# Kernel tuning notes

Hardware: AMD Instinct MI355X
Metric: run time of the kernel (lower is better)

Reference implementation:

```python
import jax, jax.numpy as jnp
import numpy as np

TEMPERATURE = 0.07


def setup_inputs() -> dict:
    key = jax.random.key(0)
    embeddings = jax.random.normal(key, (16384, 256), dtype=jnp.float32)
    return {"embeddings": embeddings}


def reference(embeddings) -> jnp.ndarray:
    # L2 normalize rows (torch F.normalize uses eps clamp 1e-12)
    norm = jnp.maximum(jnp.linalg.norm(embeddings, axis=1, keepdims=True), 1e-12)
    emb = embeddings / norm
    # [N, N] similarity, temperature-scaled logits
    logits = jnp.matmul(emb, emb.T) / TEMPERATURE
    # cross entropy against diagonal labels (labels[i] = i)
    logp = jax.nn.log_softmax(logits, axis=1)
    loss = -jnp.mean(jnp.diagonal(logp))
    return loss
```

## Files before the change

kernel.cpp:

```cpp
#include <hip/hip_runtime.h>
#include <hip/hip_bf16.h>

typedef __bf16 bf16;
typedef __attribute__((ext_vector_type(8))) __bf16 bf16x8;
typedef __attribute__((ext_vector_type(4))) __bf16 bf16x4;
typedef __attribute__((ext_vector_type(16))) float f32x16;

#define N_ROWS 16384
#define DIM 256
#define NJC 512
#define NBLKS 1024
#define NTILES 33024
#define SQK1 4.53981608f
#define LN2F 0.69314718056f

#define WS_T_OFF (N_ROWS * DIM * 2)
#define WS_D_OFF (WS_T_OFF + N_ROWS * 4)

#define GLOAD_LDS(g, l)                                        \
    __builtin_amdgcn_global_load_lds(                          \
        (const __attribute__((address_space(1))) void*)(g),    \
        (__attribute__((address_space(3))) void*)(l), 16, 0, 0)

__global__ void __launch_bounds__(256) normalize_kernel(const float* __restrict__ in,
                                                        bf16* __restrict__ out,
                                                        float* __restrict__ Tg,
                                                        float* __restrict__ Dg,
                                                        float* __restrict__ loss_out) {
    if (blockIdx.x == 0 && threadIdx.x == 0) loss_out[0] = 0.0f;
    if (blockIdx.x < 64) Tg[blockIdx.x * 256 + threadIdx.x] = 0.0f;

    const int row  = blockIdx.x * 4 + (threadIdx.x >> 6);
    const int lane = threadIdx.x & 63;
    const float4* rp = (const float4*)(in + (size_t)row * DIM);
    float4 v = rp[lane];
    float ss = v.x * v.x + v.y * v.y + v.z * v.z + v.w * v.w;
#pragma unroll
    for (int m = 1; m < 64; m <<= 1) ss += __shfl_xor(ss, m, 64);
    float inv = SQK1 / fmaxf(sqrtf(ss), 1e-12f);
    bf16x4 o;
    o[0] = (bf16)(v.x * inv);
    o[1] = (bf16)(v.y * inv);
    o[2] = (bf16)(v.z * inv);
    o[3] = (bf16)(v.w * inv);
    *(bf16x4*)(out + (size_t)row * DIM + lane * 4) = o;

    float f0 = (float)o[0], f1 = (float)o[1], f2 = (float)o[2], f3 = (float)o[3];
    float s2 = f0 * f0 + f1 * f1 + f2 * f2 + f3 * f3;
#pragma unroll
    for (int m = 1; m < 64; m <<= 1) s2 += __shfl_xor(s2, m, 64);
    if (lane == 0) Dg[row] = s2;
}

#define TREE16(R, out)                                                     \
    do {                                                                   \
        float w8[8], w4[4], w2[2], w1, g_;                                 \
        _Pragma("unroll") for (int i_ = 0; i_ < 8; ++i_) {                 \
            g_ = (lo & 16) ? R[i_] : R[i_ + 8];                            \
            w8[i_] = ((lo & 16) ? R[i_ + 8] : R[i_]) + __shfl_xor(g_, 16); \
        }                                                                  \
        _Pragma("unroll") for (int i_ = 0; i_ < 4; ++i_) {                 \
            g_ = (lo & 8) ? w8[i_] : w8[i_ + 4];                           \
            w4[i_] = ((lo & 8) ? w8[i_ + 4] : w8[i_]) + __shfl_xor(g_, 8); \
        }                                                                  \
        _Pragma("unroll") for (int i_ = 0; i_ < 2; ++i_) {                 \
            g_ = (lo & 4) ? w4[i_] : w4[i_ + 2];                           \
            w2[i_] = ((lo & 4) ? w4[i_ + 2] : w4[i_]) + __shfl_xor(g_, 4); \
        }                                                                  \
        g_ = (lo & 2) ? w2[0] : w2[1];                                     \
        w1 = ((lo & 2) ? w2[1] : w2[0]) + __shfl_xor(g_, 2);               \
        out = w1 + __shfl_xor(w1, 1);                                      \
    } while (0)

__global__ void __launch_bounds__(256, 4)
loss_kernel(const bf16* __restrict__ A, float* __restrict__ Tg) {
    __shared__ bf16 Bs0[32 * DIM];
    __shared__ bf16 Bs1[32 * DIM];

    const int tid = threadIdx.x;
    const int w  = tid >> 6;
    const int l  = tid & 63;
    const int lo = l & 31, hi = l >> 5;

    const int tbeg = (int)(((unsigned)blockIdx.x * 129u) >> 2);
    const int tend = (int)((((unsigned)blockIdx.x + 1u) * 129u) >> 2);
    const int nrem = tend - tbeg;

    int it = 0;
    while (2 * (it + 1) * (257 - (it + 1)) <= tbeg) ++it;
    int jc = 4 * it + (tbeg - 2 * it * (257 - it));

    bf16x8 af[16];
#define LOAD_AF                                                              \
    do {                                                                     \
        const bf16* ap_ = A + (size_t)(it * 128 + w * 32 + lo) * DIM + hi * 8; \
        _Pragma("unroll") for (int k_ = 0; k_ < 16; ++k_)                    \
            af[k_] = *(const volatile bf16x8*)(ap_ + k_ * 16);               \
    } while (0)
    LOAD_AF;

    float s0[16];
#pragma unroll
    for (int r = 0; r < 16; ++r) s0[r] = 0.f;

    const int s_dma = l & 31;
    const int rl    = l >> 5;
    int vo[4];
#pragma unroll
    for (int q = 0; q < 4; ++q) {
        const int c = (s_dma & 24) | ((s_dma & 7) ^ ((q * 2 + rl) & 7));
        vo[q] = rl * DIM + c * 8;
    }

    const int rbase = lo * DIM;
    const int mx7 = lo & 7;

#define ISSUE(jcn_, BUF)                                                     \
    do {                                                                     \
        const bf16* tb_ = A + (size_t)((jcn_) * 32 + w * 8) * DIM;           \
        bf16* lb_ = &BUF[(w * 8) * DIM];                                     \
        _Pragma("unroll") for (int q_ = 0; q_ < 4; ++q_) {                   \
            GLOAD_LDS(tb_ + (q_ * 2) * DIM + vo[q_],                         \
                      lb_ + (q_ * 2) * DIM);                                 \
        }                                                                    \
    } while (0)

#define FLUSH_ROWS                                                           \
    do {                                                                     \
        float tr_;                                                           \
        TREE16(s0, tr_);                                                     \
        const int r_ = (lo >> 1) & 15;                                       \
        const int rowoff_ = (r_ & 3) + 8 * (r_ >> 2) + 4 * hi;               \
        if ((l & 1) == 0)                                                    \
            atomicAdd(&Tg[it * 128 + w * 32 + rowoff_], tr_);                \
    } while (0)

    int t = 0, jcn, itn;
    bool has_next;

#define NEXT_DECODE                                                          \
    do {                                                                     \
        has_next = (t + 1 < nrem);                                           \
        if (has_next) {                                                      \
            jcn = jc + 1; itn = it;                                          \
            if (jcn == NJC) { itn = it + 1; jcn = 4 * itn; }                 \
        } else { jcn = jc; itn = it; }                                       \
    } while (0)

#define TILE_BODY(BR, BW, WN, WL)                                            \
    do {                                                                     \
        asm volatile("s_barrier" ::: "memory");                              \
        if (has_next) {                                                      \
            ISSUE(jcn, BW);                                                  \
            asm volatile("s_waitcnt vmcnt(" #WN ")" ::: "memory");           \
        } else {                                                             \
            asm volatile("s_waitcnt vmcnt(" #WL ")" ::: "memory");           \
        }                                                                    \
        asm volatile("s_barrier" ::: "memory");                              \
        f32x16 c0;                                                           \
        _Pragma("unroll") for (int r_ = 0; r_ < 16; ++r_) c0[r_] = 0.f;      \
        __builtin_amdgcn_s_setprio(1);                                       \
        _Pragma("unroll") for (int k_ = 0; k_ < 16; ++k_) {                  \
            const int cc_ = k_ * 2 + hi;                                     \
            const int slot_ = (cc_ & 24) | ((cc_ & 7) ^ mx7);                \
            bf16x8 b_ = *(const bf16x8*)&BR[rbase + slot_ * 8];              \
            c0 = __builtin_amdgcn_mfma_f32_32x32x16_bf16(af[k_], b_, c0, 0, 0, 0); \
        }                                                                    \
        __builtin_amdgcn_s_setprio(0);                                       \
        float cs_ = 0.f;                                                     \
        _Pragma("unroll") for (int r_ = 0; r_ < 16; ++r_) {                  \
            float e_ = __builtin_amdgcn_exp2f(c0[r_]);                       \
            s0[r_] += e_;                                                    \
            cs_ += e_;                                                       \
        }                                                                    \
        cs_ += __shfl_xor(cs_, 32);                                          \
         \
         \
        const float fv_ = ((jc >> 2) == it) ? 0.0f : cs_;                    \
        if (hi == 0) atomicAdd(&Tg[jc * 32 + lo], fv_);                      \
    } while (0)

#define ADVANCE                                                              \
    do {                                                                     \
        ++t;                                                                 \
        if (itn != it) {                                                     \
            FLUSH_ROWS;                                                      \
            it = itn;                                                        \
            LOAD_AF;                                                         \
            _Pragma("unroll") for (int r_ = 0; r_ < 16; ++r_) s0[r_] = 0.f;  \
        }                                                                    \
        jc = jcn;                                                            \
    } while (0)

    ISSUE(jc, Bs0);
    NEXT_DECODE;
    TILE_BODY(Bs0, Bs1, 4, 0);
    ADVANCE;
    while (t < nrem) {
        NEXT_DECODE;
        TILE_BODY(Bs1, Bs0, 5, 1);
        ADVANCE;
        if (t >= nrem) break;
        NEXT_DECODE;
        TILE_BODY(Bs0, Bs1, 5, 1);
        ADVANCE;
    }
    FLUSH_ROWS;

#undef ISSUE
#undef TILE_BODY
#undef NEXT_DECODE
#undef ADVANCE
#undef FLUSH_ROWS
#undef LOAD_AF
}

__global__ void __launch_bounds__(256) final_kernel(const float* __restrict__ Tg,
                                                    const float* __restrict__ Dg,
                                                    float* __restrict__ out) {
    __shared__ float red[4];
    const int i = blockIdx.x * 256 + threadIdx.x;
    float c = LN2F * (__log2f(Tg[i]) - Dg[i]) * (1.0f / (float)N_ROWS);
#pragma unroll
    for (int m = 1; m < 64; m <<= 1) c += __shfl_xor(c, m, 64);
    if ((threadIdx.x & 63) == 0) red[threadIdx.x >> 6] = c;
    __syncthreads();
    if (threadIdx.x == 0)
        atomicAdd(out, red[0] + red[1] + red[2] + red[3]);
}

extern "C" void kernel_launch(void* const* d_in, const int* in_sizes, int n_in,
                              void* d_out, int out_size, void* d_ws, size_t ws_size,
                              hipStream_t stream) {
    const float* emb = (const float*)d_in[0];
    float* out = (float*)d_out;
    bf16* Abf = (bf16*)d_ws;
    float* Tg = (float*)((char*)d_ws + WS_T_OFF);
    float* Dg = (float*)((char*)d_ws + WS_D_OFF);

    hipLaunchKernelGGL(normalize_kernel, dim3(N_ROWS / 4), dim3(256), 0, stream,
                       emb, Abf, Tg, Dg, out);
    hipLaunchKernelGGL(loss_kernel, dim3(NBLKS), dim3(256), 0, stream,
                       Abf, Tg);
    hipLaunchKernelGGL(final_kernel, dim3(N_ROWS / 256), dim3(256), 0, stream,
                       Tg, Dg, out);
}
```

Baseline: 156.3 us.

## Halve loss kernel waves, give each wave two 32-row A fragments

The loss kernel now runs 128 threads (2 waves) per block instead of 4. Each wave holds two 32-row A fragments and issues two MFMAs per LDS B read. This halves the shared-memory B reads per MFMA and doubles the DMA issue per wave, with the vmcnt waits adjusted to match. In exchange each wave uses many more registers, and there are fewer waves per block to hide latency.

```diff
diff --git a/kernel.cpp b/kernel.cpp
--- a/kernel.cpp
+++ b/kernel.cpp
@@ -72,7 +72,7 @@
         out = w1 + __shfl_xor(w1, 1);                                      \
     } while (0)
 
-__global__ void __launch_bounds__(256, 4)
+__global__ void __launch_bounds__(128, 2)
 loss_kernel(const bf16* __restrict__ A, float* __restrict__ Tg) {
     __shared__ bf16 Bs0[32 * DIM];
     __shared__ bf16 Bs1[32 * DIM];
@@ -90,24 +90,26 @@
     while (2 * (it + 1) * (257 - (it + 1)) <= tbeg) ++it;
     int jc = 4 * it + (tbeg - 2 * it * (257 - it));
 
-    bf16x8 af[16];
+    bf16x8 af0[16], af1[16];
 #define LOAD_AF                                                              \
     do {                                                                     \
-        const bf16* ap_ = A + (size_t)(it * 128 + w * 32 + lo) * DIM + hi * 8; \
-        _Pragma("unroll") for (int k_ = 0; k_ < 16; ++k_)                    \
-            af[k_] = *(const volatile bf16x8*)(ap_ + k_ * 16);               \
+        const bf16* ap_ = A + (size_t)(it * 128 + w * 64 + lo) * DIM + hi * 8; \
+        _Pragma("unroll") for (int k_ = 0; k_ < 16; ++k_) {                  \
+            af0[k_] = *(const volatile bf16x8*)(ap_ + k_ * 16);              \
+            af1[k_] = *(const volatile bf16x8*)(ap_ + 32 * DIM + k_ * 16);   \
+        }                                                                    \
     } while (0)
     LOAD_AF;
 
-    float s0[16];
-#pragma unroll
-    for (int r = 0; r < 16; ++r) s0[r] = 0.f;
+    float s0a[16], s0b[16];
+#pragma unroll
+    for (int r = 0; r < 16; ++r) { s0a[r] = 0.f; s0b[r] = 0.f; }
 
     const int s_dma = l & 31;
     const int rl    = l >> 5;
-    int vo[4];
-#pragma unroll
-    for (int q = 0; q < 4; ++q) {
+    int vo[8];
+#pragma unroll
+    for (int q = 0; q < 8; ++q) {
         const int c = (s_dma & 24) | ((s_dma & 7) ^ ((q * 2 + rl) & 7));
         vo[q] = rl * DIM + c * 8;
     }
@@ -117,9 +119,9 @@
 
 #define ISSUE(jcn_, BUF)                                                     \
     do {                                                                     \
-        const bf16* tb_ = A + (size_t)((jcn_) * 32 + w * 8) * DIM;           \
-        bf16* lb_ = &BUF[(w * 8) * DIM];                                     \
-        _Pragma("unroll") for (int q_ = 0; q_ < 4; ++q_) {                   \
+        const bf16* tb_ = A + (size_t)((jcn_) * 32 + w * 16) * DIM;          \
+        bf16* lb_ = &BUF[(w * 16) * DIM];                                    \
+        _Pragma("unroll") for (int q_ = 0; q_ < 8; ++q_) {                   \
             GLOAD_LDS(tb_ + (q_ * 2) * DIM + vo[q_],                         \
                       lb_ + (q_ * 2) * DIM);                                 \
         }                                                                    \
@@ -127,12 +129,15 @@
 
 #define FLUSH_ROWS                                                           \
     do {                                                                     \
-        float tr_;                                                           \
-        TREE16(s0, tr_);                                                     \
+        float tra_, trb_;                                                    \
+        TREE16(s0a, tra_);                                                   \
+        TREE16(s0b, trb_);                                                   \
         const int r_ = (lo >> 1) & 15;                                       \
         const int rowoff_ = (r_ & 3) + 8 * (r_ >> 2) + 4 * hi;               \
-        if ((l & 1) == 0)                                                    \
-            atomicAdd(&Tg[it * 128 + w * 32 + rowoff_], tr_);                \
+        if ((l & 1) == 0) {                                                  \
+            atomicAdd(&Tg[it * 128 + w * 64 + rowoff_], tra_);               \
+            atomicAdd(&Tg[it * 128 + w * 64 + 32 + rowoff_], trb_);          \
+        }                                                                    \
     } while (0)
 
     int t = 0, jcn, itn;
@@ -157,21 +162,29 @@
             asm volatile("s_waitcnt vmcnt(" #WL ")" ::: "memory");           \
         }                                                                    \
         asm volatile("s_barrier" ::: "memory");                              \
-        f32x16 c0;                                                           \
-        _Pragma("unroll") for (int r_ = 0; r_ < 16; ++r_) c0[r_] = 0.f;      \
+        f32x16 c0a, c0b;                                                     \
+        _Pragma("unroll") for (int r_ = 0; r_ < 16; ++r_) {                  \
+            c0a[r_] = 0.f; c0b[r_] = 0.f;                                    \
+        }                                                                    \
         __builtin_amdgcn_s_setprio(1);                                       \
         _Pragma("unroll") for (int k_ = 0; k_ < 16; ++k_) {                  \
             const int cc_ = k_ * 2 + hi;                                     \
             const int slot_ = (cc_ & 24) | ((cc_ & 7) ^ mx7);                \
             bf16x8 b_ = *(const bf16x8*)&BR[rbase + slot_ * 8];              \
-            c0 = __builtin_amdgcn_mfma_f32_32x32x16_bf16(af[k_], b_, c0, 0, 0, 0); \
+            c0a = __builtin_amdgcn_mfma_f32_32x32x16_bf16(af0[k_], b_, c0a, 0, 0, 0); \
+            c0b = __builtin_amdgcn_mfma_f32_32x32x16_bf16(af1[k_], b_, c0b, 0, 0, 0); \
         }                                                                    \
         __builtin_amdgcn_s_setprio(0);                                       \
         float cs_ = 0.f;                                                     \
         _Pragma("unroll") for (int r_ = 0; r_ < 16; ++r_) {                  \
-            float e_ = __builtin_amdgcn_exp2f(c0[r_]);                       \
-            s0[r_] += e_;                                                    \
-            cs_ += e_;                                                       \
+            float ea_ = __builtin_amdgcn_exp2f(c0a[r_]);                     \
+            s0a[r_] += ea_;                                                  \
+            cs_ += ea_;                                                      \
+        }                                                                    \
+        _Pragma("unroll") for (int r_ = 0; r_ < 16; ++r_) {                  \
+            float eb_ = __builtin_amdgcn_exp2f(c0b[r_]);                     \
+            s0b[r_] += eb_;                                                  \
+            cs_ += eb_;                                                      \
         }                                                                    \
         cs_ += __shfl_xor(cs_, 32);                                          \
          \
@@ -187,22 +200,24 @@
             FLUSH_ROWS;                                                      \
             it = itn;                                                        \
             LOAD_AF;                                                         \
-            _Pragma("unroll") for (int r_ = 0; r_ < 16; ++r_) s0[r_] = 0.f;  \
+            _Pragma("unroll") for (int r_ = 0; r_ < 16; ++r_) {              \
+                s0a[r_] = 0.f; s0b[r_] = 0.f;                                \
+            }                                                                \
         }                                                                    \
         jc = jcn;                                                            \
     } while (0)
 
     ISSUE(jc, Bs0);
     NEXT_DECODE;
-    TILE_BODY(Bs0, Bs1, 4, 0);
+    TILE_BODY(Bs0, Bs1, 8, 0);
     ADVANCE;
     while (t < nrem) {
         NEXT_DECODE;
-        TILE_BODY(Bs1, Bs0, 5, 1);
+        TILE_BODY(Bs1, Bs0, 9, 1);
         ADVANCE;
         if (t >= nrem) break;
         NEXT_DECODE;
-        TILE_BODY(Bs0, Bs1, 5, 1);
+        TILE_BODY(Bs0, Bs1, 9, 1);
         ADVANCE;
     }
     FLUSH_ROWS;
@@ -240,7 +255,7 @@
 
     hipLaunchKernelGGL(normalize_kernel, dim3(N_ROWS / 4), dim3(256), 0, stream,
                        emb, Abf, Tg, Dg, out);
-    hipLaunchKernelGGL(loss_kernel, dim3(NBLKS), dim3(256), 0, stream,
+    hipLaunchKernelGGL(loss_kernel, dim3(NBLKS), dim3(128), 0, stream,
                        Abf, Tg);
     hipLaunchKernelGGL(final_kernel, dim3(N_ROWS / 256), dim3(256), 0, stream,
                        Tg, Dg, out);
```

New measurement: 220.6 us. +41.1%, slower.

## Software-pipeline exp2 epilogue of previous tile under current tile's MFMAs

Applied to the files above, without the earlier changes.

Restructures the tile loop so two accumulator sets alternate. The exp2 and sum epilogue of the previous tile is interleaved with the MFMA chain of the current tile, hiding the transcendental and VALU work behind matrix ops. The next row block's A fragments are also prefetched earlier (non-volatile loads), and the deferred row and column sums are flushed one step late. Launch bounds are relaxed from 4 to 1 waves per EU so the extra accumulator registers fit, which may lower occupancy.

```diff
diff --git a/kernel.cpp b/kernel.cpp
--- a/kernel.cpp
+++ b/kernel.cpp
@@ -72,7 +72,7 @@
         out = w1 + __shfl_xor(w1, 1);                                      \
     } while (0)
 
-__global__ void __launch_bounds__(256, 4)
+__global__ void __launch_bounds__(256, 1)
 loss_kernel(const bf16* __restrict__ A, float* __restrict__ Tg) {
     __shared__ bf16 Bs0[32 * DIM];
     __shared__ bf16 Bs1[32 * DIM];
@@ -91,13 +91,13 @@
     int jc = 4 * it + (tbeg - 2 * it * (257 - it));
 
     bf16x8 af[16];
-#define LOAD_AF                                                              \
-    do {                                                                     \
-        const bf16* ap_ = A + (size_t)(it * 128 + w * 32 + lo) * DIM + hi * 8; \
+#define LOAD_AF(ITX)                                                         \
+    do {                                                                     \
+        const bf16* ap_ = A + (size_t)((ITX) * 128 + w * 32 + lo) * DIM + hi * 8; \
         _Pragma("unroll") for (int k_ = 0; k_ < 16; ++k_)                    \
-            af[k_] = *(const volatile bf16x8*)(ap_ + k_ * 16);               \
-    } while (0)
-    LOAD_AF;
+            af[k_] = *(const bf16x8*)(ap_ + k_ * 16);                        \
+    } while (0)
+    LOAD_AF(it);
 
     float s0[16];
 #pragma unroll
@@ -125,17 +125,18 @@
         }                                                                    \
     } while (0)
 
-#define FLUSH_ROWS                                                           \
+#define FLUSH_ROWS(ITP)                                                      \
     do {                                                                     \
         float tr_;                                                           \
         TREE16(s0, tr_);                                                     \
         const int r_ = (lo >> 1) & 15;                                       \
         const int rowoff_ = (r_ & 3) + 8 * (r_ >> 2) + 4 * hi;               \
         if ((l & 1) == 0)                                                    \
-            atomicAdd(&Tg[it * 128 + w * 32 + rowoff_], tr_);                \
+            atomicAdd(&Tg[(ITP) * 128 + w * 32 + rowoff_], tr_);             \
     } while (0)
 
     int t = 0, jcn, itn;
+    int itP = it, jcP = jc;
     bool has_next;
 
 #define NEXT_DECODE                                                          \
@@ -147,7 +148,7 @@
         } else { jcn = jc; itn = it; }                                       \
     } while (0)
 
-#define TILE_BODY(BR, BW, WN, WL)                                            \
+#define STEP_SYNC(BW, WN, WL)                                                \
     do {                                                                     \
         asm volatile("s_barrier" ::: "memory");                              \
         if (has_next) {                                                      \
@@ -157,60 +158,89 @@
             asm volatile("s_waitcnt vmcnt(" #WL ")" ::: "memory");           \
         }                                                                    \
         asm volatile("s_barrier" ::: "memory");                              \
-        f32x16 c0;                                                           \
-        _Pragma("unroll") for (int r_ = 0; r_ < 16; ++r_) c0[r_] = 0.f;      \
-        __builtin_amdgcn_s_setprio(1);                                       \
+    } while (0)
+
+#define STEP_ADVANCE                                                         \
+    do {                                                                     \
+        itP = it; jcP = jc;                                                  \
+        if (itn != it) LOAD_AF(itn);                                         \
+        it = itn; jc = jcn; ++t;                                             \
+    } while (0)
+
+#define STEP_NOEPI(BR, BW, CN, WN, WL)                                       \
+    do {                                                                     \
+        NEXT_DECODE;                                                         \
+        STEP_SYNC(BW, WN, WL);                                               \
+        _Pragma("unroll") for (int r_ = 0; r_ < 16; ++r_) CN[r_] = 0.f;      \
         _Pragma("unroll") for (int k_ = 0; k_ < 16; ++k_) {                  \
             const int cc_ = k_ * 2 + hi;                                     \
             const int slot_ = (cc_ & 24) | ((cc_ & 7) ^ mx7);                \
             bf16x8 b_ = *(const bf16x8*)&BR[rbase + slot_ * 8];              \
-            c0 = __builtin_amdgcn_mfma_f32_32x32x16_bf16(af[k_], b_, c0, 0, 0, 0); \
-        }                                                                    \
-        __builtin_amdgcn_s_setprio(0);                                       \
+            CN = __builtin_amdgcn_mfma_f32_32x32x16_bf16(af[k_], b_, CN, 0, 0, 0); \
+        }                                                                    \
+        STEP_ADVANCE;                                                        \
+    } while (0)
+
+#define STEP_EPI(BR, BW, CN, CO, WN, WL)                                     \
+    do {                                                                     \
+        NEXT_DECODE;                                                         \
+        STEP_SYNC(BW, WN, WL);                                               \
+        _Pragma("unroll") for (int r_ = 0; r_ < 16; ++r_) CN[r_] = 0.f;      \
+        float cs_ = 0.f;                                                     \
+        _Pragma("unroll") for (int k_ = 0; k_ < 16; ++k_) {                  \
+            const int cc_ = k_ * 2 + hi;                                     \
+            const int slot_ = (cc_ & 24) | ((cc_ & 7) ^ mx7);                \
+            bf16x8 b_ = *(const bf16x8*)&BR[rbase + slot_ * 8];              \
+            CN = __builtin_amdgcn_mfma_f32_32x32x16_bf16(af[k_], b_, CN, 0, 0, 0); \
+            float e0_ = __builtin_amdgcn_exp2f(CO[2 * k_]);                  \
+            float e1_ = __builtin_amdgcn_exp2f(CO[2 * k_ + 1]);              \
+            s0[2 * k_]     += e0_;                                           \
+            s0[2 * k_ + 1] += e1_;                                           \
+            cs_ += e0_ + e1_;                                                \
+        }                                                                    \
+        cs_ += __shfl_xor(cs_, 32);                                          \
+        const float fv_ = ((jcP >> 2) == itP) ? 0.0f : cs_;                  \
+        if (hi == 0) atomicAdd(&Tg[jcP * 32 + lo], fv_);                     \
+        if (itP != it) {                                                     \
+            FLUSH_ROWS(itP);                                                 \
+            _Pragma("unroll") for (int r_ = 0; r_ < 16; ++r_) s0[r_] = 0.f;  \
+        }                                                                    \
+        STEP_ADVANCE;                                                        \
+    } while (0)
+
+#define DRAIN(CO)                                                            \
+    do {                                                                     \
         float cs_ = 0.f;                                                     \
         _Pragma("unroll") for (int r_ = 0; r_ < 16; ++r_) {                  \
-            float e_ = __builtin_amdgcn_exp2f(c0[r_]);                       \
+            float e_ = __builtin_amdgcn_exp2f(CO[r_]);                       \
             s0[r_] += e_;                                                    \
             cs_ += e_;                                                       \
         }                                                                    \
         cs_ += __shfl_xor(cs_, 32);                                          \
-         \
-         \
-        const float fv_ = ((jc >> 2) == it) ? 0.0f : cs_;                    \
-        if (hi == 0) atomicAdd(&Tg[jc * 32 + lo], fv_);                      \
-    } while (0)
-
-#define ADVANCE                                                              \
-    do {                                                                     \
-        ++t;                                                                 \
-        if (itn != it) {                                                     \
-            FLUSH_ROWS;                                                      \
-            it = itn;                                                        \
-            LOAD_AF;                                                         \
-            _Pragma("unroll") for (int r_ = 0; r_ < 16; ++r_) s0[r_] = 0.f;  \
-        }                                                                    \
-        jc = jcn;                                                            \
-    } while (0)
+        const float fv_ = ((jcP >> 2) == itP) ? 0.0f : cs_;                  \
+        if (hi == 0) atomicAdd(&Tg[jcP * 32 + lo], fv_);                     \
+    } while (0)
+
+    f32x16 cA, cB;
 
     ISSUE(jc, Bs0);
-    NEXT_DECODE;
-    TILE_BODY(Bs0, Bs1, 4, 0);
-    ADVANCE;
+    STEP_NOEPI(Bs0, Bs1, cA, 4, 0);
+    STEP_EPI(Bs1, Bs0, cB, cA, 4, 0);
     while (t < nrem) {
-        NEXT_DECODE;
-        TILE_BODY(Bs1, Bs0, 5, 1);
-        ADVANCE;
+        STEP_EPI(Bs0, Bs1, cA, cB, 5, 1);
         if (t >= nrem) break;
-        NEXT_DECODE;
-        TILE_BODY(Bs0, Bs1, 5, 1);
-        ADVANCE;
+        STEP_EPI(Bs1, Bs0, cB, cA, 5, 1);
     }
-    FLUSH_ROWS;
+    if (nrem & 1) DRAIN(cA); else DRAIN(cB);
+    FLUSH_ROWS(itP);
 
 #undef ISSUE
-#undef TILE_BODY
+#undef STEP_SYNC
+#undef STEP_ADVANCE
+#undef STEP_NOEPI
+#undef STEP_EPI
+#undef DRAIN
 #undef NEXT_DECODE
-#undef ADVANCE
 #undef FLUSH_ROWS
 #undef LOAD_AF
 }
```

Measured after the change: 157.6 us. No clear change (+0.8%).
